# Kernel optimization log

Measured on AMD Instinct MI355X. Metric: run time of the kernel, lower is better.

Reference implementation:

```python
import jax, jax.numpy as jnp
import numpy as np

QLEN, MLEN, BSZ, DM, NH, DH, DI = 512, 512, 8, 1024, 16, 64, 4096
KLEN = QLEN + MLEN
EPS = 1e-5
NEG = -1e30


def layer_norm(x, g, b):
    mu = jnp.mean(x, axis=-1, keepdims=True)
    var = jnp.mean(jnp.square(x - mu), axis=-1, keepdims=True)
    return (x - mu) * jax.lax.rsqrt(var + EPS) * g + b


def rel_shift(x):
    # x: [qlen, rlen, bsz, n_head] -> Transformer-XL relative shift
    q, r, b, n = x.shape
    zp = jnp.zeros((q, 1, b, n), x.dtype)
    xp = jnp.concatenate([zp, x], axis=1).reshape(r + 1, q, b, n)
    return xp[1:].reshape(q, r, b, n)


def setup_inputs() -> dict:
    key = jax.random.key(0)
    ks = jax.random.split(key, 12)
    inp = {
        "w": jax.random.normal(ks[0], (QLEN, BSZ, DM), jnp.float32),
        "r": jax.random.normal(ks[1], (KLEN, DM), jnp.float32),
        "mems": jax.random.normal(ks[2], (MLEN, BSZ, DM), jnp.float32),
        "w_qkv": jax.random.normal(ks[3], (DM, 3 * NH * DH), jnp.float32) * 0.02,
        "w_r": jax.random.normal(ks[4], (DM, NH * DH), jnp.float32) * 0.02,
        "w_o": jax.random.normal(ks[5], (NH * DH, DM), jnp.float32) * 0.02,
        "r_w_bias": jax.random.normal(ks[6], (NH, DH), jnp.float32) * 0.02,
        "r_r_bias": jax.random.normal(ks[7], (NH, DH), jnp.float32) * 0.02,
        "ln1_g": jnp.ones((DM,), jnp.float32),
        "ln1_b": jnp.zeros((DM,), jnp.float32),
        "ff_w1": jax.random.normal(ks[8], (DM, DI), jnp.float32) * 0.02,
        "ff_b1": jnp.zeros((DI,), jnp.float32),
        "ff_w2": jax.random.normal(ks[9], (DI, DM), jnp.float32) * 0.02,
        "ff_b2": jnp.zeros((DM,), jnp.float32),
        "ln2_g": jnp.ones((DM,), jnp.float32),
        "ln2_b": jnp.zeros((DM,), jnp.float32),
    }
    # causal mask with memory: query i (global pos MLEN+i) cannot attend to j > MLEN+i
    i = jnp.arange(QLEN)[:, None]
    j = jnp.arange(KLEN)[None, :]
    inp["attn_mask"] = j > (i + MLEN)
    return inp


def reference(w, r, mems, attn_mask, w_qkv, w_r, w_o, r_w_bias, r_r_bias,
              ln1_g, ln1_b, ff_w1, ff_b1, ff_w2, ff_b2, ln2_g, ln2_b):
    qlen, bsz = w.shape[0], w.shape[1]
    scale = 1.0 / (DH ** 0.5)
    cat = jnp.concatenate([mems, w], axis=0)                 # [klen, b, d]
    klen = cat.shape[0]
    heads = cat @ w_qkv                                      # [klen, b, 3*H*D]
    hq, hk, hv = jnp.split(heads, 3, axis=-1)
    hq = hq[-qlen:].reshape(qlen, bsz, NH, DH)
    hk = hk.reshape(klen, bsz, NH, DH)
    hv = hv.reshape(klen, bsz, NH, DH)
    r_head_k = (r @ w_r).reshape(klen, NH, DH)               # [rlen, H, D]

    AC = jnp.einsum('ibnd,jbnd->ijbn', hq + r_w_bias, hk)
    BD = rel_shift(jnp.einsum('ibnd,jnd->ijbn', hq + r_r_bias, r_head_k))
    score = (AC + BD) * scale                                # [q, k, b, h]
    score = jnp.where(attn_mask[:, :, None, None], NEG, score)
    prob = jax.nn.softmax(score, axis=1)
    vec = jnp.einsum('ijbn,jbnd->ibnd', prob, hv).reshape(qlen, bsz, NH * DH)
    attn_out = vec @ w_o
    h = layer_norm(w + attn_out, ln1_g, ln1_b)               # post-LN
    ff = jax.nn.relu(h @ ff_w1 + ff_b1) @ ff_w2 + ff_b2
    return layer_norm(h + ff, ln2_g, ln2_b)
```

## Files before the change

### kernel.cpp

```cpp
#include <hip/hip_runtime.h>
#include <hip/hip_bf16.h>

#define QLEN 512
#define MLEN 512
#define KLEN 1024
#define BSZ 8
#define DM 1024
#define NH 16
#define DH 64
#define DI 4096
#define NEGF (-1e30f)

typedef unsigned short u16;
typedef __attribute__((ext_vector_type(8))) short short8;
typedef __attribute__((ext_vector_type(4))) short s16x4;
typedef __attribute__((ext_vector_type(4))) float f32x4;

__device__ __forceinline__ float bf2f(u16 u) {
    union { unsigned i; float f; } x; x.i = ((unsigned)u) << 16; return x.f;
}
__device__ __forceinline__ u16 f2bf(float f) {
    __hip_bfloat16 h = __float2bfloat16(f);
    return *reinterpret_cast<u16*>(&h);
}
__device__ __forceinline__ float4 ldg4(const float* p) {
    return *reinterpret_cast<const float4*>(p);
}
__device__ __forceinline__ void gload16(const void* g, void* l) {
    __builtin_amdgcn_global_load_lds(
        (const __attribute__((address_space(1))) void*)g,
        (__attribute__((address_space(3))) void*)l, 16, 0, 0);
}

__global__ __launch_bounds__(256) void cast2_kernel(
    const float* __restrict__ a, const float* __restrict__ b, int splitE,
    u16* __restrict__ out, int n)
{
    int idx = (blockIdx.x * 256 + threadIdx.x) * 4;
    if (idx >= n) return;
    const float* src = (idx < splitE) ? (a + idx) : (b + (idx - splitE));
    float4 v = ldg4(src);
    u16 o[4] = { f2bf(v.x), f2bf(v.y), f2bf(v.z), f2bf(v.w) };
    *reinterpret_cast<uint2*>(&out[idx]) = *reinterpret_cast<uint2*>(o);
}

__device__ __forceinline__ void tr32(
    const float* __restrict__ W, u16* __restrict__ WT, int K, int N, int k0, int n0)
{
    __shared__ float tile[32][33];
    const int tx = threadIdx.x & 31, ty = threadIdx.x >> 5;
    #pragma unroll
    for (int j = 0; j < 4; ++j)
        tile[ty + j * 8][tx] = W[(size_t)(k0 + ty + j * 8) * N + n0 + tx];
    __syncthreads();
    #pragma unroll
    for (int j = 0; j < 4; ++j)
        WT[(size_t)(n0 + ty + j * 8) * K + k0 + tx] = f2bf(tile[tx][ty + j * 8]);
}

__global__ __launch_bounds__(256) void transpose_all(
    const float* __restrict__ w_qkv, u16* __restrict__ qkvT,
    const float* __restrict__ w_r,   u16* __restrict__ wrT,
    const float* __restrict__ w_o,   u16* __restrict__ woT,
    const float* __restrict__ ffw1,  u16* __restrict__ f1T,
    const float* __restrict__ ffw2,  u16* __restrict__ f2T)
{
    int id = blockIdx.x;
    if (id < 3072)       { int l = id;        tr32(w_qkv, qkvT, 1024, 3072, (l / 96) * 32, (l % 96) * 32); }
    else if (id < 4096)  { int l = id - 3072; tr32(w_r,   wrT,  1024, 1024, (l / 32) * 32, (l % 32) * 32); }
    else if (id < 5120)  { int l = id - 4096; tr32(w_o,   woT,  1024, 1024, (l / 32) * 32, (l % 32) * 32); }
    else if (id < 9216)  { int l = id - 5120; tr32(ffw1,  f1T,  1024, 4096, (l / 128) * 32, (l % 128) * 32); }
    else                 { int l = id - 9216; tr32(ffw2,  f2T,  4096, 1024, (l / 32) * 32, (l % 32) * 32); }
}

__global__ __launch_bounds__(256) void v_transpose(
    const u16* __restrict__ heads, u16* __restrict__ Vg)
{
    const int bn = blockIdx.x;
    const int b = bn >> 4, n = bn & 15;
    const int kt = blockIdx.y;
    const int t = threadIdx.x;
    __shared__ u16 L[64 * 64];

    #pragma unroll
    for (int rep = 0; rep < 2; ++rep) {
        int idx = t + rep * 256;
        int key = idx >> 3, dc = (idx & 7) * 8;
        short8 v = *reinterpret_cast<const short8*>(
            &heads[((size_t)((kt * 64 + key) * BSZ + b)) * 3072 + 2048 + n * 64 + dc]);
        *reinterpret_cast<short8*>((char*)L + key * 128 + ((dc * 2) ^ ((key & 7) << 4))) = v;
    }
    __syncthreads();
    #pragma unroll
    for (int rep = 0; rep < 2; ++rep) {
        int idx = t + rep * 256;
        int d = idx >> 3, kc = (idx & 7) * 8;
        short8 o;
        #pragma unroll
        for (int e = 0; e < 8; ++e)
            o[e] = *(const short*)((char*)L + (kc + e) * 128 + ((d * 2) ^ (((kc + e) & 7) << 4)));
        *reinterpret_cast<short8*>(&Vg[((size_t)(bn * 64 + d)) * KLEN + kt * 64 + kc]) = o;
    }
}

template<bool BIAS, bool RELU, bool OUTBF>
__global__ __launch_bounds__(256) void gemm_mfma(
    const u16* __restrict__ A, const u16* __restrict__ BT,
    const float* __restrict__ bias,
    float* __restrict__ Cf, u16* __restrict__ Cb,
    int M, int N, int K, int lda, int ldb)
{
    __shared__ u16 As[128 * 64];
    __shared__ u16 Bs[128 * 64];
    const int bm = blockIdx.y * 128, bn = blockIdx.x * 128;
    const int z = blockIdx.z;
    A  += (size_t)z * K;
    BT += (size_t)z * K;
    const size_t zoff = (size_t)z * M * N;
    const int t = threadIdx.x;
    const int w = t >> 6, l = t & 63, lg = l >> 4, lq = l & 15;
    const int wm = (w >> 1) * 64, wn = (w & 1) * 64;
    const int r8 = l >> 3, slot = l & 7;
    const int gcol = (slot * 16) ^ (r8 << 4);

    f32x4 acc[4][4];
    #pragma unroll
    for (int x = 0; x < 4; ++x)
        #pragma unroll
        for (int y = 0; y < 4; ++y)
            acc[x][y] = (f32x4){0.f, 0.f, 0.f, 0.f};

    const int swzr = (lq & 7) << 4;

    for (int k0 = 0; k0 < K; k0 += 64) {
        __syncthreads();
        #pragma unroll
        for (int it = 0; it < 4; ++it) {
            const int base_row = w * 8 + it * 32;
            gload16((const char*)A + (((size_t)(bm + base_row + r8) * lda + k0) << 1) + gcol,
                    (char*)As + base_row * 128);
            gload16((const char*)BT + (((size_t)(bn + base_row + r8) * ldb + k0) << 1) + gcol,
                    (char*)Bs + base_row * 128);
        }
        __syncthreads();
        #pragma unroll
        for (int ks = 0; ks < 2; ++ks) {
            const int cb = (ks * 64 + 16 * lg) ^ swzr;
            short8 af[4], bf_[4];
            #pragma unroll
            for (int x = 0; x < 4; ++x)
                af[x] = *reinterpret_cast<const short8*>((char*)As + (wm + 16 * x + lq) * 128 + cb);
            #pragma unroll
            for (int y = 0; y < 4; ++y)
                bf_[y] = *reinterpret_cast<const short8*>((char*)Bs + (wn + 16 * y + lq) * 128 + cb);
            #pragma unroll
            for (int x = 0; x < 4; ++x)
                #pragma unroll
                for (int y = 0; y < 4; ++y)
                    acc[x][y] = __builtin_amdgcn_mfma_f32_16x16x32_bf16(af[x], bf_[y], acc[x][y], 0, 0, 0);
        }
    }
    #pragma unroll
    for (int x = 0; x < 4; ++x) {
        #pragma unroll
        for (int y = 0; y < 4; ++y) {
            const int col = bn + wn + 16 * y + lq;
            #pragma unroll
            for (int r = 0; r < 4; ++r) {
                const int row = bm + wm + 16 * x + 4 * lg + r;
                float v = acc[x][y][r];
                if constexpr (BIAS) { if (z == 0) v += bias[col]; }
                if constexpr (RELU) v = fmaxf(v, 0.f);
                if constexpr (OUTBF) Cb[zoff + (size_t)row * N + col] = f2bf(v);
                else                 Cf[zoff + (size_t)row * N + col] = v;
            }
        }
    }
}

__global__ __launch_bounds__(512, 4) void attn_mfma(
    const u16* __restrict__ heads,
    const u16* __restrict__ Vg,
    const u16* __restrict__ rhk,
    const float* __restrict__ rwb, const float* __restrict__ rrb,
    u16* __restrict__ vec)
{
    const int b = blockIdx.x >> 4;
    const int n = blockIdx.x & 15;
    const int i0 = (3 - blockIdx.y) * 128;
    const int t = threadIdx.x;
    const int w = t >> 6;
    const int l = t & 63;
    const int lg = l >> 4, lq = l & 15;
    const int r8 = l >> 3, sl = l & 7;

    __shared__ u16 Ks[64 * 64];
    __shared__ u16 Vt[64 * 64];
    __shared__ u16 Rs[192 * 64];
    __shared__ u16 SbO[8 * 16 * 84];
    __shared__ u16 Ps[8 * 16 * 64];

    u16* SbW = SbO + w * 16 * 84;
    u16* PsW = Ps + w * 16 * 64;
    const int swzr = (lq & 7) << 4;
    const int stg_swz = (sl * 16) ^ (r8 << 4);

    short8 qw[2], qr[2];
    {
        const int qrow = i0 + 16 * w + lq;
        const size_t gbase = ((size_t)((MLEN + qrow) * BSZ + b)) * 3072 + n * 64;
        #pragma unroll
        for (int ks = 0; ks < 2; ++ks) {
            short8 qv = *reinterpret_cast<const short8*>(&heads[gbase + ks * 32 + 8 * lg]);
            short8 xw, xr;
            #pragma unroll
            for (int e = 0; e < 8; ++e) {
                float f = bf2f((u16)qv[e]);
                int d = ks * 32 + 8 * lg + e;
                xw[e] = (short)f2bf(f + rwb[n * 64 + d]);
                xr[e] = (short)f2bf(f + rrb[n * 64 + d]);
            }
            qw[ks] = xw; qr[ks] = xr;
        }
    }

    float m_run = NEGF, l_run = 0.f;
    f32x4 acc[4];
    #pragma unroll
    for (int df = 0; df < 4; ++df) acc[df] = (f32x4){0.f, 0.f, 0.f, 0.f};

    const int s0 = 112 - 16 * w;
    const int ntiles = i0 / 64 + 10;

    for (int tile = 0; tile < ntiles; ++tile) {
        const int j0 = tile << 6;
        __syncthreads();
        gload16((const char*)heads
                    + (((size_t)((j0 + w * 8 + r8) * BSZ + b)) * 3072 + 1024 + n * 64) * 2
                    + stg_swz,
                (char*)Ks + w * 1024);
        gload16((const char*)Vg
                    + (((size_t)(blockIdx.x * 64 + w * 8 + r8)) * KLEN + j0) * 2
                    + stg_swz,
                (char*)Vt + w * 1024);
        const int obase = j0 - i0 + 384;
        #pragma unroll
        for (int pass = 0; pass < 3; ++pass) {
            int row = pass * 64 + w * 8 + r8;
            int o = obase + row;
            o = o > (KLEN - 1) ? (KLEN - 1) : o;
            gload16((const char*)rhk + ((size_t)o * 1024 + n * 64) * 2 + stg_swz,
                    (char*)Rs + pass * 8192 + w * 1024);
        }
        __syncthreads();

        __builtin_amdgcn_s_setprio(1);
        #pragma unroll
        for (int ff = 0; ff < 5; ++ff) {
            f32x4 d = (f32x4){0.f, 0.f, 0.f, 0.f};
            #pragma unroll
            for (int ks = 0; ks < 2; ++ks) {
                short8 a = *reinterpret_cast<const short8*>(
                    (char*)Rs + (s0 + 16 * ff + lq) * 128 + ((ks * 64 + 16 * lg) ^ swzr));
                d = __builtin_amdgcn_mfma_f32_16x16x32_bf16(a, qr[ks], d, 0, 0, 0);
            }
            s16x4 pk;
            #pragma unroll
            for (int r = 0; r < 4; ++r) pk[r] = (short)f2bf(d[r]);
            *reinterpret_cast<s16x4*>(&SbW[lq * 84 + 16 * ff + 4 * lg]) = pk;
        }
        f32x4 dac[4];
        #pragma unroll
        for (int f = 0; f < 4; ++f) {
            f32x4 d = (f32x4){0.f, 0.f, 0.f, 0.f};
            #pragma unroll
            for (int ks = 0; ks < 2; ++ks) {
                short8 a = *reinterpret_cast<const short8*>(
                    (char*)Ks + (16 * f + lq) * 128 + ((ks * 64 + 16 * lg) ^ swzr));
                d = __builtin_amdgcn_mfma_f32_16x16x32_bf16(a, qw[ks], d, 0, 0, 0);
            }
            dac[f] = d;
        }
        __builtin_amdgcn_s_setprio(0);

        const bool fullTile = (i0 + 16 * w + MLEN - j0) >= 63;
        float sv[4][4];
        float mx = NEGF;
        if (fullTile) {
            #pragma unroll
            for (int f = 0; f < 4; ++f)
                #pragma unroll
                for (int r = 0; r < 4; ++r) {
                    int k = 16 * f + 4 * lg + r;
                    float bd = bf2f(SbW[lq * 84 + k - lq + 15]);
                    float x = (dac[f][r] + bd) * 0.125f;
                    sv[f][r] = x;
                    mx = fmaxf(mx, x);
                }
        } else {
            const int bound = i0 + 16 * w + lq + MLEN - j0;
            #pragma unroll
            for (int f = 0; f < 4; ++f)
                #pragma unroll
                for (int r = 0; r < 4; ++r) {
                    int k = 16 * f + 4 * lg + r;
                    float bd = bf2f(SbW[lq * 84 + k - lq + 15]);
                    float x = (k <= bound) ? (dac[f][r] + bd) * 0.125f : NEGF;
                    sv[f][r] = x;
                    mx = fmaxf(mx, x);
                }
        }
        mx = fmaxf(mx, __shfl_xor(mx, 16));
        mx = fmaxf(mx, __shfl_xor(mx, 32));
        float m_new = fmaxf(m_run, mx);
        float alpha = __expf(m_run - m_new);
        float ps = 0.f;
        #pragma unroll
        for (int f = 0; f < 4; ++f) {
            s16x4 pk;
            #pragma unroll
            for (int r = 0; r < 4; ++r) {
                float p = __expf(sv[f][r] - m_new);
                ps += p;
                pk[r] = (short)f2bf(p);
            }
            *reinterpret_cast<s16x4*>(
                (char*)PsW + lq * 128 + (((4 * f + lg) ^ ((lq & 7) << 1)) << 3)) = pk;
        }
        ps += __shfl_xor(ps, 16);
        ps += __shfl_xor(ps, 32);
        l_run = l_run * alpha + ps;
        m_run = m_new;

        float alr[4];
        #pragma unroll
        for (int r = 0; r < 4; ++r) alr[r] = __shfl(alpha, 20 * lg + r);
        __builtin_amdgcn_s_setprio(1);
        #pragma unroll
        for (int df = 0; df < 4; ++df) {
            f32x4 a = acc[df];
            #pragma unroll
            for (int r = 0; r < 4; ++r) a[r] *= alr[r];
            #pragma unroll
            for (int ks = 0; ks < 2; ++ks) {
                short8 pa = *reinterpret_cast<const short8*>(
                    (char*)PsW + lq * 128 + ((ks * 64 + 16 * lg) ^ swzr));
                short8 vb = *reinterpret_cast<const short8*>(
                    (char*)Vt + (16 * df + lq) * 128 + ((ks * 64 + 16 * lg) ^ swzr));
                a = __builtin_amdgcn_mfma_f32_16x16x32_bf16(pa, vb, a, 0, 0, 0);
            }
            acc[df] = a;
        }
        __builtin_amdgcn_s_setprio(0);
    }

    float inv[4];
    #pragma unroll
    for (int r = 0; r < 4; ++r) inv[r] = 1.f / __shfl(l_run, 20 * lg + r);
    #pragma unroll
    for (int df = 0; df < 4; ++df) {
        #pragma unroll
        for (int r = 0; r < 4; ++r) {
            const int il = 16 * w + 4 * lg + r;
            float o = acc[df][r] * inv[r];
            vec[((size_t)((i0 + il) * BSZ + b)) * DM + n * 64 + 16 * df + lq] = f2bf(o);
        }
    }
}

template<int NRES, bool WB>
__global__ __launch_bounds__(256) void ln_res_kernel(
    const float* __restrict__ x, const float* __restrict__ res,
    const float* __restrict__ res2,
    const float* __restrict__ g, const float* __restrict__ bta,
    float* __restrict__ out, u16* __restrict__ outb)
{
    const int row = blockIdx.x;
    const int t = threadIdx.x;
    const int lane = t & 63, wv = t >> 6;
    __shared__ float red0[4], red1[4];

    float4 a = ldg4(&x[(size_t)row * DM + t * 4]);
    float4 b = ldg4(&res[(size_t)row * DM + t * 4]);
    float v0 = a.x + b.x, v1 = a.y + b.y, v2 = a.z + b.z, v3 = a.w + b.w;
    if constexpr (NRES == 2) {
        float4 c = ldg4(&res2[(size_t)row * DM + t * 4]);
        v0 += c.x; v1 += c.y; v2 += c.z; v3 += c.w;
    }
    float s = v0 + v1 + v2 + v3;
    #pragma unroll
    for (int o = 32; o; o >>= 1) s += __shfl_xor(s, o);
    if (lane == 0) red0[wv] = s;
    __syncthreads();
    float mu = (red0[0] + red0[1] + red0[2] + red0[3]) * (1.f / DM);
    float d0 = v0 - mu, d1 = v1 - mu, d2 = v2 - mu, d3 = v3 - mu;
    float q = d0*d0 + d1*d1 + d2*d2 + d3*d3;
    #pragma unroll
    for (int o = 32; o; o >>= 1) q += __shfl_xor(q, o);
    if (lane == 0) red1[wv] = q;
    __syncthreads();
    float var = (red1[0] + red1[1] + red1[2] + red1[3]) * (1.f / DM);
    float rs = rsqrtf(var + 1e-5f);
    float4 gv = ldg4(&g[t * 4]);
    float4 bv = ldg4(&bta[t * 4]);
    float o0 = d0 * rs * gv.x + bv.x;
    float o1 = d1 * rs * gv.y + bv.y;
    float o2 = d2 * rs * gv.z + bv.z;
    float o3 = d3 * rs * gv.w + bv.w;
    float4 o4 = make_float4(o0, o1, o2, o3);
    *reinterpret_cast<float4*>(&out[(size_t)row * DM + t * 4]) = o4;
    if constexpr (WB) {
        u16 ob[4] = { f2bf(o0), f2bf(o1), f2bf(o2), f2bf(o3) };
        *reinterpret_cast<uint2*>(&outb[(size_t)row * DM + t * 4]) = *reinterpret_cast<uint2*>(ob);
    }
}

extern "C" void kernel_launch(void* const* d_in, const int* in_sizes, int n_in,
                              void* d_out, int out_size, void* d_ws, size_t ws_size,
                              hipStream_t stream) {
    const float* w     = (const float*)d_in[0];
    const float* r     = (const float*)d_in[1];
    const float* mems  = (const float*)d_in[2];
    const float* w_qkv = (const float*)d_in[3];
    const float* w_r   = (const float*)d_in[4];
    const float* w_o   = (const float*)d_in[5];
    const float* rwb   = (const float*)d_in[6];
    const float* rrb   = (const float*)d_in[7];
    const float* ln1g  = (const float*)d_in[8];
    const float* ln1b  = (const float*)d_in[9];
    const float* ffw1  = (const float*)d_in[10];
    const float* ffb1  = (const float*)d_in[11];
    const float* ffw2  = (const float*)d_in[12];
    const float* ffb2  = (const float*)d_in[13];
    const float* ln2g  = (const float*)d_in[14];
    const float* ln2b  = (const float*)d_in[15];
    (void)in_sizes; (void)n_in; (void)out_size; (void)ws_size;

    char* p = (char*)d_ws;
    auto alloc = [&](size_t bytes) { char* q = p; p += (bytes + 255) & ~(size_t)255; return q; };
    u16* catB   = (u16*)alloc((size_t)8192 * 1024 * 2);
    u16* rB     = (u16*)alloc((size_t)1024 * 1024 * 2);
    u16* qkvT   = (u16*)alloc((size_t)3072 * 1024 * 2);
    u16* wrT    = (u16*)alloc((size_t)1024 * 1024 * 2);
    u16* woT    = (u16*)alloc((size_t)1024 * 1024 * 2);
    u16* f1T    = (u16*)alloc((size_t)4096 * 1024 * 2);
    u16* f2T    = (u16*)alloc((size_t)1024 * 4096 * 2);
    u16* heads  = (u16*)alloc((size_t)8192 * 3072 * 2);
    u16* rhk    = (u16*)alloc((size_t)1024 * 1024 * 2);
    u16* vec    = (u16*)alloc((size_t)4096 * 1024 * 2);
    u16* hB     = (u16*)alloc((size_t)4096 * 1024 * 2);
    u16* ff1    = (u16*)alloc((size_t)4096 * 4096 * 2);
    float* hF   = (float*)alloc((size_t)4096 * 1024 * 4);

    u16* Vg = catB;
    float* attn_out = (float*)ff1;
    float* ff2 = (float*)heads;
    float* outp = (float*)d_out;

    cast2_kernel<<<8192, 256, 0, stream>>>(mems, w, 4096 * 1024, catB, 8192 * 1024);
    cast2_kernel<<<1024, 256, 0, stream>>>(r, r, 1024 * 1024, rB, 1024 * 1024);
    transpose_all<<<13312, 256, 0, stream>>>(w_qkv, qkvT, w_r, wrT, w_o, woT,
                                             ffw1, f1T, ffw2, f2T);

    gemm_mfma<false, false, true><<<dim3(24, 64), 256, 0, stream>>>(
        catB, qkvT, nullptr, nullptr, heads, 8192, 3072, 1024, 1024, 1024);
    v_transpose<<<dim3(128, 16), 256, 0, stream>>>(heads, Vg);
    gemm_mfma<false, false, true><<<dim3(8, 8), 256, 0, stream>>>(
        rB, wrT, nullptr, nullptr, rhk, 1024, 1024, 1024, 1024, 1024);
    attn_mfma<<<dim3(BSZ * NH, QLEN / 128), 512, 0, stream>>>(
        heads, Vg, rhk, rwb, rrb, vec);
    gemm_mfma<false, false, false><<<dim3(8, 32, 2), 256, 0, stream>>>(
        vec, woT, nullptr, attn_out, nullptr, 4096, 1024, 512, 1024, 1024);
    ln_res_kernel<2, true><<<4096, 256, 0, stream>>>(
        w, attn_out, attn_out + (size_t)4096 * 1024, ln1g, ln1b, hF, hB);
    gemm_mfma<true, true, true><<<dim3(32, 32), 256, 0, stream>>>(
        hB, f1T, ffb1, nullptr, ff1, 4096, 4096, 1024, 1024, 1024);
    gemm_mfma<true, false, false><<<dim3(8, 32, 2), 256, 0, stream>>>(
        ff1, f2T, ffb2, ff2, nullptr, 4096, 1024, 2048, 4096, 4096);
    ln_res_kernel<2, false><<<4096, 256, 0, stream>>>(
        hF, ff2, ff2 + (size_t)4096 * 1024, ln2g, ln2b, outp, nullptr);
}
```

Baseline: 344.5 us.

## Add triple-buffered 256x128 GEMM kernel for QKV and FFN projections

Adds a gemm_deep kernel with 512 threads, a 256x128 output tile and a three-stage LDS ring filled by async global-to-LDS loads. Loads run two tiles ahead and are gated with explicit vmcnt waits, and MFMA issue is wrapped in s_setprio. It replaces the older GEMM for the QKV, FF1 and FF2 projections to hide global memory latency and raise reuse per block. In exchange it uses 144KB of LDS per block and launches fewer, larger blocks, which can lower occupancy and leave the grid less evenly spread across CUs.

Result: faster. 328.4 us (-4.7%).

```diff
diff --git a/kernel.cpp b/kernel.cpp
--- a/kernel.cpp
+++ b/kernel.cpp
@@ -160,6 +160,99 @@
                     acc[x][y] = __builtin_amdgcn_mfma_f32_16x16x32_bf16(af[x], bf_[y], acc[x][y], 0, 0, 0);
         }
     }
+    #pragma unroll
+    for (int x = 0; x < 4; ++x) {
+        #pragma unroll
+        for (int y = 0; y < 4; ++y) {
+            const int col = bn + wn + 16 * y + lq;
+            #pragma unroll
+            for (int r = 0; r < 4; ++r) {
+                const int row = bm + wm + 16 * x + 4 * lg + r;
+                float v = acc[x][y][r];
+                if constexpr (BIAS) { if (z == 0) v += bias[col]; }
+                if constexpr (RELU) v = fmaxf(v, 0.f);
+                if constexpr (OUTBF) Cb[zoff + (size_t)row * N + col] = f2bf(v);
+                else                 Cf[zoff + (size_t)row * N + col] = v;
+            }
+        }
+    }
+}
+
+template<bool BIAS, bool RELU, bool OUTBF>
+__global__ __launch_bounds__(512, 2) void gemm_deep(
+    const u16* __restrict__ A, const u16* __restrict__ BT,
+    const float* __restrict__ bias,
+    float* __restrict__ Cf, u16* __restrict__ Cb,
+    int M, int N, int K, int lda, int ldb)
+{
+    __shared__ u16 lds[3 * 24576];
+    const int bm = blockIdx.y * 256, bn = blockIdx.x * 128;
+    const int z = blockIdx.z;
+    A  += (size_t)z * K;
+    BT += (size_t)z * K;
+    const size_t zoff = (size_t)z * M * N;
+    const int t = threadIdx.x;
+    const int w = t >> 6, l = t & 63, lg = l >> 4, lq = l & 15;
+    const int wm = (w >> 1) * 64;
+    const int wn = (w & 1) * 64;
+    const int srow = t >> 3, slot = t & 7;
+    const int gcol = (slot * 16) ^ ((srow & 7) << 4);
+    const int swzr = (lq & 7) << 4;
+
+    auto stage_tile = [&](int kt, int buf) {
+        const int k0 = kt * 64;
+        char* Ab = (char*)lds + buf * 49152 + w * 1024;
+        char* Bb = (char*)lds + buf * 49152 + 32768 + w * 1024;
+        #pragma unroll
+        for (int i = 0; i < 4; ++i)
+            gload16((const char*)A + (((size_t)(bm + i * 64 + srow) * lda + k0) << 1) + gcol,
+                    Ab + i * 8192);
+        #pragma unroll
+        for (int i = 0; i < 2; ++i)
+            gload16((const char*)BT + (((size_t)(bn + i * 64 + srow) * ldb + k0) << 1) + gcol,
+                    Bb + i * 8192);
+    };
+
+    f32x4 acc[4][4];
+    #pragma unroll
+    for (int x = 0; x < 4; ++x)
+        #pragma unroll
+        for (int y = 0; y < 4; ++y)
+            acc[x][y] = (f32x4){0.f, 0.f, 0.f, 0.f};
+
+    const int NT = K >> 6;
+    stage_tile(0, 0);
+    stage_tile(1, 1);
+
+    for (int kt = 0; kt < NT; ++kt) {
+        if (kt < NT - 1) asm volatile("s_waitcnt vmcnt(6)" ::: "memory");
+        else             asm volatile("s_waitcnt vmcnt(0)" ::: "memory");
+        __builtin_amdgcn_s_barrier();
+        __builtin_amdgcn_sched_barrier(0);
+        if (kt + 2 < NT) stage_tile(kt + 2, (kt + 2) % 3);
+
+        const char* Ab = (const char*)lds + (kt % 3) * 49152;
+        const char* Bb = Ab + 32768;
+        #pragma unroll
+        for (int ks = 0; ks < 2; ++ks) {
+            const int cb = (ks * 64 + 16 * lg) ^ swzr;
+            short8 af[4], bf_[4];
+            #pragma unroll
+            for (int x = 0; x < 4; ++x)
+                af[x] = *reinterpret_cast<const short8*>(Ab + (wm + 16 * x + lq) * 128 + cb);
+            #pragma unroll
+            for (int y = 0; y < 4; ++y)
+                bf_[y] = *reinterpret_cast<const short8*>(Bb + (wn + 16 * y + lq) * 128 + cb);
+            __builtin_amdgcn_s_setprio(1);
+            #pragma unroll
+            for (int x = 0; x < 4; ++x)
+                #pragma unroll
+                for (int y = 0; y < 4; ++y)
+                    acc[x][y] = __builtin_amdgcn_mfma_f32_16x16x32_bf16(af[x], bf_[y], acc[x][y], 0, 0, 0);
+            __builtin_amdgcn_s_setprio(0);
+        }
+    }
+
     #pragma unroll
     for (int x = 0; x < 4; ++x) {
         #pragma unroll
@@ -462,7 +555,7 @@
     transpose_all<<<13312, 256, 0, stream>>>(w_qkv, qkvT, w_r, wrT, w_o, woT,
                                              ffw1, f1T, ffw2, f2T);
 
-    gemm_mfma<false, false, true><<<dim3(24, 64), 256, 0, stream>>>(
+    gemm_deep<false, false, true><<<dim3(24, 32), 512, 0, stream>>>(
         catB, qkvT, nullptr, nullptr, heads, 8192, 3072, 1024, 1024, 1024);
     v_transpose<<<dim3(128, 16), 256, 0, stream>>>(heads, Vg);
     gemm_mfma<false, false, true><<<dim3(8, 8), 256, 0, stream>>>(
@@ -473,9 +566,9 @@
         vec, woT, nullptr, attn_out, nullptr, 4096, 1024, 512, 1024, 1024);
     ln_res_kernel<2, true><<<4096, 256, 0, stream>>>(
         w, attn_out, attn_out + (size_t)4096 * 1024, ln1g, ln1b, hF, hB);
-    gemm_mfma<true, true, true><<<dim3(32, 32), 256, 0, stream>>>(
+    gemm_deep<true, true, true><<<dim3(32, 16), 512, 0, stream>>>(
         hB, f1T, ffb1, nullptr, ff1, 4096, 4096, 1024, 1024, 1024);
-    gemm_mfma<true, false, false><<<dim3(8, 32, 2), 256, 0, stream>>>(
+    gemm_deep<true, false, false><<<dim3(8, 16, 2), 512, 0, stream>>>(
         ff1, f2T, ffb2, ff2, nullptr, 4096, 1024, 2048, 4096, 4096);
     ln_res_kernel<2, false><<<4096, 256, 0, stream>>>(
         hF, ff2, ff2 + (size_t)4096 * 1024, ln2g, ln2b, outp, nullptr);
```
